# Performance work log

Hardware: AMD Instinct MI355X
Metric: run time of the kernel (lower is better)

The kernel has to match this reference:

```python
import jax, jax.numpy as jnp
from jax import lax
import numpy as np

B, N, D_MODEL = 4, 2048, 768
D_INNER = 1536      # int(2.0 * d_model)
DT_RANK = 48        # ceil(768 / 16)
EPS = 1e-5


def setup_inputs() -> dict:
    key = jax.random.key(0)
    ks = jax.random.split(key, 9)
    x = jax.random.normal(ks[0], (B, N, D_MODEL), jnp.float32)
    # BFS order: a permutation of node ids
    sorted_index = jax.random.permutation(ks[1], N).astype(jnp.int32)
    # parent BFS position of node at BFS position i, must be < i; root (i=0) has -1
    pos = jnp.arange(N)
    r = jax.random.randint(ks[2], (N,), 0, N)
    sorted_parent = jnp.where(pos == 0, -1, r % jnp.maximum(pos, 1)).astype(jnp.int32)
    s = 0.02
    in_proj_w = jax.random.normal(ks[3], (D_MODEL, 2 * D_INNER), jnp.float32) * s
    x_proj_w = jax.random.normal(ks[4], (D_INNER, DT_RANK + 2), jnp.float32) * s
    dt_proj_w = jax.random.normal(ks[5], (DT_RANK, D_INNER), jnp.float32) * (DT_RANK ** -0.5)
    # dt bias init: softplus^{-1}(dt) with dt ~ LogUniform(1e-3, 1e-1)
    dt = jnp.exp(jax.random.uniform(ks[6], (D_INNER,)) * (np.log(0.1) - np.log(0.001)) + np.log(0.001))
    dt_proj_b = (dt + jnp.log(-jnp.expm1(-dt))).astype(jnp.float32)
    A_log = jnp.zeros((D_INNER,), jnp.float32)   # log(A=1) per original init (d_state=1)
    D_param = jnp.ones((D_INNER,), jnp.float32)
    ln_gamma = jnp.ones((D_INNER,), jnp.float32)
    ln_beta = jnp.zeros((D_INNER,), jnp.float32)
    out_proj_w = jax.random.normal(ks[7], (D_INNER, D_MODEL), jnp.float32) * s
    return dict(x=x, sorted_index=sorted_index, sorted_parent=sorted_parent,
                in_proj_w=in_proj_w, x_proj_w=x_proj_w, dt_proj_w=dt_proj_w,
                dt_proj_b=dt_proj_b, A_log=A_log, D_param=D_param,
                ln_gamma=ln_gamma, ln_beta=ln_beta, out_proj_w=out_proj_w)


def _tree_ssm_recurrence(dBx, dA, sorted_index, sorted_parent):
    """h[bfs i] = dA[node(i)] * h[parent_bfs(i)] + dBx[node(i)]. Inputs (B,N,Di) node-major."""
    b, n, di = dBx.shape
    dA_bfs = jnp.take(dA, sorted_index, axis=1)    # (B,N,Di) in BFS order
    dBx_bfs = jnp.take(dBx, sorted_index, axis=1)

    def step(h_buf, inp):
        t, par, dA_t, dBx_t = inp                   # dA_t/dBx_t: (B,Di)
        h_par = h_buf[:, jnp.maximum(par, 0)]       # (B,Di) gather at parent BFS pos
        h_par = jnp.where(par < 0, jnp.zeros_like(h_par), h_par)
        h_t = dA_t * h_par + dBx_t
        return h_buf.at[:, t].set(h_t), h_t

    xs = (jnp.arange(n), sorted_parent,
          dA_bfs.transpose(1, 0, 2), dBx_bfs.transpose(1, 0, 2))
    _, h_bfs = lax.scan(step, jnp.zeros((b, n, di), dBx.dtype), xs)
    # scatter BFS-order states back to node-id order
    h = jnp.zeros((b, n, di), dBx.dtype).at[:, sorted_index].set(h_bfs.transpose(1, 0, 2))
    return h


def reference(x, sorted_index, sorted_parent, in_proj_w, x_proj_w, dt_proj_w,
              dt_proj_b, A_log, D_param, ln_gamma, ln_beta, out_proj_w):
    xz = x @ in_proj_w                              # (B,N,2*Di)
    x_inner, z = jnp.split(xz, 2, axis=-1)
    z = jax.nn.silu(z)
    x_dbl = x_inner @ x_proj_w                      # (B,N,dt_rank+2)
    dt_lr, B_ssm, C_ssm = (x_dbl[..., :DT_RANK], x_dbl[..., DT_RANK:DT_RANK + 1],
                           x_dbl[..., DT_RANK + 1:DT_RANK + 2])
    dt = jax.nn.softplus(dt_lr @ dt_proj_w + dt_proj_b)  # (B,N,Di)
    As = -jnp.exp(A_log)                            # (Di,) negative
    dA = jnp.exp(dt * As)                           # (B,N,Di) in (0,1)
    dBx = dt * B_ssm * x_inner                      # (B,N,Di)
    h = _tree_ssm_recurrence(dBx, dA, sorted_index, sorted_parent)
    y = h * C_ssm + D_param * x_inner               # (B,N,Di)
    mu = jnp.mean(y, axis=-1, keepdims=True)
    var = jnp.mean(jnp.square(y - mu), axis=-1, keepdims=True)
    y = (y - mu) * lax.rsqrt(var + EPS) * ln_gamma + ln_beta
    y = y * z
    return y @ out_proj_w                           # (B,N,D)
```

## Files before the change

kernel.cpp:

```cpp
#include <hip/hip_runtime.h>
#include <math.h>


#define ROWS 8192
#define DIN 1536
#define DMOD 768
#define NSEQ 2048
#define DTR 48

typedef __bf16 bfrag __attribute__((ext_vector_type(8)));
typedef float f4 __attribute__((ext_vector_type(4)));

__device__ __forceinline__ unsigned short f2bf(float f) {
  unsigned int u = __float_as_uint(f);
  unsigned int r = (u + 0x7fffu + ((u >> 16) & 1u)) >> 16;
  return (unsigned short)r;
}
__device__ __forceinline__ float bf2f(unsigned short h) {
  return __uint_as_float(((unsigned int)h) << 16);
}

__device__ __forceinline__ void gld_lds16(const void* g, void* l) {
  __builtin_amdgcn_global_load_lds((const __attribute__((address_space(1))) void*)g,
                                   (__attribute__((address_space(3))) void*)l, 16, 0, 0);
}

__device__ __forceinline__ void barx() {
  asm volatile("" ::: "memory");
  __builtin_amdgcn_s_barrier();
  asm volatile("" ::: "memory");
}

template <int MODE, int NCOLS>
__global__ __launch_bounds__(512, 2) void gemm_dp(
    const unsigned short* __restrict__ A, const unsigned short* __restrict__ Bt,
    void* __restrict__ C0v, void* __restrict__ C1v, int K, int ldc) {
  __shared__ unsigned short lds[2][(128 + 192) * 64];
  const int tid = threadIdx.x;
  const int w = tid >> 6, l = tid & 63;
  const int quad = l >> 4, l16 = l & 15;
  const int wr = w >> 2, wc = w & 3;
  const int h = blockIdx.x + gridDim.x * blockIdx.y;
  const int chunk = (gridDim.x * gridDim.y) >> 3;
  const int swz = (h & 7) * chunk + (h >> 3);
  const int row0 = (swz / NCOLS) * 128, col0 = (swz % NCOLS) * 192;
  const int nt = K >> 6;

  const int srow = tid >> 3;
  const int schunk = ((tid & 7) ^ (srow & 7)) * 8;
  const unsigned short* aS = A + (size_t)(row0 + srow) * K + schunk;
  const unsigned short* bS = Bt + (size_t)(col0 + srow) * K + schunk;

#define STG_A(bufi, q, kt)                                     \
  gld_lds16(aS + (size_t)((q) * 64) * K + (size_t)(kt) * 64,   \
            (char*)&lds[bufi][(q) * 4096] + w * 1024)
#define STG_B(bufi, q, kt)                                     \
  gld_lds16(bS + (size_t)((q) * 64) * K + (size_t)(kt) * 64,   \
            (char*)&lds[bufi][8192 + (q) * 4096] + w * 1024)

  const int arow = (wr * 64 + l16) * 64;
  const int brow = (wc * 48 + l16) * 64;
  int cs[2];
  cs[0] = (quad ^ (l16 & 7)) * 8;
  cs[1] = ((4 + quad) ^ (l16 & 7)) * 8;

#define RDA(m, ks) (*(const bfrag*)(const void*)(LA + arow + (m) * 1024 + cs[ks]))
#define RDB(n, ks) (*(const bfrag*)(const void*)(LB + brow + (n) * 1024 + cs[ks]))

  f4 acc[4][3];
#pragma unroll
  for (int m = 0; m < 4; m++)
#pragma unroll
    for (int n = 0; n < 3; n++) acc[m][n] = (f4){0.f, 0.f, 0.f, 0.f};

  const int kt1 = (nt > 1) ? 1 : 0;
#pragma unroll
  for (int q = 0; q < 2; q++) STG_A(0, q, 0);
#pragma unroll
  for (int q = 0; q < 3; q++) STG_B(0, q, 0);
#pragma unroll
  for (int q = 0; q < 2; q++) STG_A(1, q, kt1);
#pragma unroll
  for (int q = 0; q < 3; q++) STG_B(1, q, kt1);
  asm volatile("s_waitcnt vmcnt(5)" ::: "memory");
  barx();

  for (int t = 0; t < nt; ++t) {
    const int b = t & 1;
    const unsigned short* LA = &lds[b][0];
    const unsigned short* LB = &lds[b][8192];
    const int kA = (t + 2 < nt) ? (t + 2) : (nt - 1);
    bfrag af[4][2], bfr[3][2];

#pragma unroll
    for (int m = 0; m < 4; m++) {
      af[m][0] = RDA(m, 0);
      af[m][1] = RDA(m, 1);
    }
#pragma unroll
    for (int n = 0; n < 3; n++) {
      bfr[n][0] = RDB(n, 0);
      bfr[n][1] = RDB(n, 1);
    }
    asm volatile("s_waitcnt lgkmcnt(0)" ::: "memory");
    barx();
    STG_A(b, 0, kA);
    STG_A(b, 1, kA);
    STG_B(b, 0, kA);
    STG_B(b, 1, kA);
    STG_B(b, 2, kA);
    __builtin_amdgcn_s_setprio(1);
#pragma unroll
    for (int m = 0; m < 4; m++)
#pragma unroll
      for (int n = 0; n < 3; n++) {
        acc[m][n] = __builtin_amdgcn_mfma_f32_16x16x32_bf16(af[m][0], bfr[n][0], acc[m][n], 0, 0, 0);
        acc[m][n] = __builtin_amdgcn_mfma_f32_16x16x32_bf16(af[m][1], bfr[n][1], acc[m][n], 0, 0, 0);
      }
    __builtin_amdgcn_s_setprio(0);
    asm volatile("s_waitcnt vmcnt(5)" ::: "memory");
    barx();
  }
  asm volatile("s_waitcnt vmcnt(0)" ::: "memory");

#undef STG_A
#undef STG_B
#undef RDA
#undef RDB

  if (MODE == 0) {
    float* C0 = (float*)C0v;
    const int cb = col0 + wc * 48 + l16;
#pragma unroll
    for (int m = 0; m < 4; m++) {
      const int rb = row0 + wr * 64 + m * 16 + quad * 4;
#pragma unroll
      for (int n = 0; n < 3; n++)
#pragma unroll
        for (int r = 0; r < 4; r++)
          C0[(size_t)(rb + r) * ldc + cb + n * 16] = acc[m][n][r];
    }
  } else {
    const bool is_z = (col0 >= DIN);
    unsigned short* dst = is_z ? (unsigned short*)C1v : (unsigned short*)C0v;
    const int cb = col0 + wc * 48 + l16 - (is_z ? DIN : 0);
#pragma unroll
    for (int m = 0; m < 4; m++) {
      const int rb = row0 + wr * 64 + m * 16 + quad * 4;
#pragma unroll
      for (int n = 0; n < 3; n++)
#pragma unroll
        for (int r = 0; r < 4; r++) {
          float v = acc[m][n][r];
          if (is_z) v = v / (1.f + __expf(-v));
          dst[(size_t)(rb + r) * DIN + cb + n * 16] = f2bf(v);
        }
    }
  }
}

__global__ __launch_bounds__(1024) void prep1_kernel(
    const int* __restrict__ sidx, const int* __restrict__ spar,
    int* __restrict__ SLOT_PACK, int* __restrict__ SLOTINV,
    int* __restrict__ LSTART, int* __restrict__ NLEV,
    const float* __restrict__ x, unsigned short* __restrict__ Xbf,
    const float* __restrict__ dtw, unsigned short* __restrict__ DTWb,
    const float* __restrict__ A_log, float* __restrict__ negA) {
  const int bi = blockIdx.x;
  const int tid = threadIdx.x;
  if (bi == 0) {
    __shared__ int par[2048], idx[2048], ancA[2048], ancB[2048], rnkA[2048], rnkB[2048];
    __shared__ int dmax;
    for (int i = tid; i < 2048; i += 1024) {
      const int p = spar[i];
      par[i] = p;
      idx[i] = sidx[i];
      ancA[i] = (p < 0) ? -1 : p;
      rnkA[i] = (p < 0) ? 0 : 1;
    }
    if (tid == 0) dmax = 0;
    __syncthreads();
    for (int r = 0; r < 11; r++) {
      int* ca = (r & 1) ? ancB : ancA;
      int* cr = (r & 1) ? rnkB : rnkA;
      int* na = (r & 1) ? ancA : ancB;
      int* nr = (r & 1) ? rnkA : rnkB;
      for (int i = tid; i < 2048; i += 1024) {
        const int a = ca[i], rv = cr[i];
        if (a >= 0) {
          nr[i] = rv + cr[a];
          na[i] = ca[a];
        } else {
          nr[i] = rv;
          na[i] = a;
        }
      }
      __syncthreads();
    }
    for (int i = tid; i < 2048; i += 1024) ancA[i] = 0;
    __syncthreads();
    for (int i = tid; i < 2048; i += 1024) {
      atomicAdd(&ancA[rnkB[i]], 1);
      atomicMax(&dmax, rnkB[i]);
    }
    __syncthreads();
    for (int s = 0; s < 11; s++) {
      const int off = 1 << s;
      int* cur = (s & 1) ? ancB : ancA;
      int* nxt = (s & 1) ? ancA : ancB;
      for (int i = tid; i < 2048; i += 1024) {
        int v = cur[i];
        if (i >= off) v += cur[i - off];
        nxt[i] = v;
      }
      __syncthreads();
    }
    for (int i = tid; i < 2049; i += 1024) {
      const int v = (i == 0) ? 0 : ancB[i - 1];
      LSTART[i] = v;
      if (i < 2048) rnkA[i] = v;
    }
    if (tid == 0) NLEV[0] = dmax + 1;
    __syncthreads();
    for (int i = tid; i < 2048; i += 1024) {
      const int d = rnkB[i];
      const int slot = atomicAdd(&rnkA[d], 1);
      const int node = idx[i];
      const int p = par[i];
      const int pn = (p < 0) ? -1 : idx[p];
      SLOT_PACK[slot] = node | ((pn + 1) << 12);
      SLOTINV[node] = slot;
    }
  } else if (bi < 1 + 1536) {
    const int i = ((bi - 1) * 1024 + tid) * 4;
    const float4 v = *(const float4*)(x + i);
    union { unsigned short h[4]; uint2 u; } pk;
    pk.h[0] = f2bf(v.x);
    pk.h[1] = f2bf(v.y);
    pk.h[2] = f2bf(v.z);
    pk.h[3] = f2bf(v.w);
    *(uint2*)(Xbf + i) = pk.u;
  } else if (bi < 1 + 1536 + 96) {
    const int i = (bi - 1537) * 1024 + tid;
    const int d = i >> 6, k = i & 63;
    DTWb[i] = (k < 48) ? f2bf(dtw[(size_t)k * DIN + d]) : (unsigned short)0;
  } else {
    const int i = (bi - 1633) * 1024 + tid;
    if (i < DIN) negA[i] = -__expf(A_log[i]);
  }
}

__global__ __launch_bounds__(256) void prep2_kernel(
    const float* __restrict__ W1, unsigned short* __restrict__ W1t,
    const float* __restrict__ W2, unsigned short* __restrict__ W2t) {
  __shared__ float t[32][33];
  int idx = blockIdx.x;
  const float* W;
  unsigned short* Wt;
  int K, N, n0, k0;
  if (idx < 2304) {
    W = W1; Wt = W1t; K = DMOD; N = 2 * DIN;
    n0 = (idx % 96) * 32; k0 = (idx / 96) * 32;
  } else {
    idx -= 2304;
    W = W2; Wt = W2t; K = DIN; N = DMOD;
    n0 = (idx % 24) * 32; k0 = (idx / 24) * 32;
  }
  const int tx = threadIdx.x & 31, ty = threadIdx.x >> 5;
  for (int i = ty; i < 32; i += 8) t[i][tx] = W[(size_t)(k0 + i) * N + n0 + tx];
  __syncthreads();
  for (int i = ty; i < 32; i += 8)
    Wt[(size_t)(n0 + i) * K + k0 + tx] = f2bf(t[tx][i]);
}

__global__ __launch_bounds__(256) void cwprep_kernel(
    const float* __restrict__ W1, const float* __restrict__ xpw,
    unsigned short* __restrict__ CWt) {
  const int tid = threadIdx.x;
  const int kk = tid >> 6, lane = tid & 63;
  const int k = blockIdx.x * 4 + kk;
  float acc[50];
#pragma unroll
  for (int c = 0; c < 50; c++) acc[c] = 0.f;
  const float* wrow = W1 + (size_t)k * (2 * DIN);
  for (int j = lane; j < DIN; j += 64) {
    const float wv = wrow[j];
    const float* xr = xpw + (size_t)j * 50;
#pragma unroll
    for (int c = 0; c < 50; c++) acc[c] = fmaf(wv, xr[c], acc[c]);
  }
#pragma unroll
  for (int c = 0; c < 50; c++) {
#pragma unroll
    for (int off = 32; off >= 1; off >>= 1) acc[c] += __shfl_down(acc[c], off);
  }
  if (lane == 0) {
#pragma unroll
    for (int c = 0; c < 50; c++) CWt[(size_t)c * DMOD + k] = f2bf(acc[c]);
  }
  if (tid < 56) {
    const int c = 50 + (tid >> 2);
    const int kz = blockIdx.x * 4 + (tid & 3);
    CWt[(size_t)c * DMOD + kz] = 0;
  }
}

__global__ __launch_bounds__(256) void xdbl2_mfma(
    const unsigned short* __restrict__ Xbf, const unsigned short* __restrict__ CWt,
    unsigned short* __restrict__ DTLRb, float* __restrict__ BCv,
    float* __restrict__ CCv) {
  __shared__ unsigned short As[64 * 32];
  __shared__ unsigned short Bs[64 * 32];
  const int tid = threadIdx.x;
  const int w = tid >> 6, l = tid & 63;
  const int quad = l >> 4, l16 = l & 15;
  const int h = blockIdx.x;
  const int swz = (h & 7) * 16 + (h >> 3);
  const int row0 = swz * 64;

  f4 acc[4];
#pragma unroll
  for (int j = 0; j < 4; j++) acc[j] = (f4){0.f, 0.f, 0.f, 0.f};

  const int srow = w * 16 + (l >> 2);
  const int kcol = (((l & 3) ^ ((l >> 2) & 3)) * 8);
  const int qs = (quad ^ (l16 & 3)) * 8;

  for (int c = 0; c < 24; c++) {
    const int k0 = c * 32;
    gld_lds16(Xbf + (size_t)(row0 + srow) * DMOD + k0 + kcol,
              (char*)As + w * 1024);
    gld_lds16(CWt + (size_t)srow * DMOD + k0 + kcol, (char*)Bs + w * 1024);
    __syncthreads();
    bfrag af, bf[4];
    af = *(const bfrag*)(const void*)(As + (w * 16 + l16) * 32 + qs);
#pragma unroll
    for (int j = 0; j < 4; j++)
      bf[j] = *(const bfrag*)(const void*)(Bs + (j * 16 + l16) * 32 + qs);
#pragma unroll
    for (int j = 0; j < 4; j++)
      acc[j] = __builtin_amdgcn_mfma_f32_16x16x32_bf16(af, bf[j], acc[j], 0, 0, 0);
    __syncthreads();
  }

#pragma unroll
  for (int j = 0; j < 4; j++) {
    const int col = j * 16 + l16;
#pragma unroll
    for (int r = 0; r < 4; r++) {
      const int row = row0 + w * 16 + quad * 4 + r;
      const float v = acc[j][r];
      DTLRb[(size_t)row * 64 + col] = f2bf(v);
      if (col == 48) BCv[row] = v;
      else if (col == 49) CCv[row] = v;
    }
  }
}

__global__ __launch_bounds__(256) void dt_gemm(
    const unsigned short* __restrict__ DTLRb, const unsigned short* __restrict__ DTWb,
    const float* __restrict__ bias, const float* __restrict__ negA,
    const float* __restrict__ BCv, const unsigned short* __restrict__ XI,
    const int* __restrict__ SLOTINV,
    unsigned short* __restrict__ DAp, unsigned short* __restrict__ DBXp) {
  __shared__ unsigned short As[2][64 * 32];
  __shared__ unsigned short Bs[2][128 * 32];
  __shared__ int sinv[64];
  __shared__ float bcs[64];
  const int tid = threadIdx.x;
  const int w = tid >> 6, l = tid & 63;
  const int quad = l >> 4, l16 = l & 15;
  const int wrow = (w >> 1) * 32, wcol = (w & 1) * 64;
  const int h = blockIdx.x + 12 * blockIdx.y;
  const int swz = (h & 7) * 192 + (h >> 3);
  const int row0 = (swz / 12) * 64, col0 = (swz % 12) * 128;
  const int p0 = row0 & (NSEQ - 1);
  const int bbase = row0 & ~(NSEQ - 1);
  const int srow = w * 16 + (l >> 2);
  const int koff = (((l & 3) ^ ((l >> 2) & 3)) * 8);
  const int qs = (quad ^ (l16 & 3)) * 8;

#pragma unroll
  for (int c = 0; c < 2; c++) {
    gld_lds16(DTLRb + (size_t)(row0 + srow) * 64 + c * 32 + koff,
              (char*)As[c] + w * 1024);
#pragma unroll
    for (int r = 0; r < 2; r++)
      gld_lds16(DTWb + (size_t)(col0 + srow + r * 64) * 64 + c * 32 + koff,
                (char*)Bs[c] + r * 4096 + w * 1024);
  }
  if (tid < 64) {
    sinv[tid] = SLOTINV[p0 + tid];
    bcs[tid] = BCv[row0 + tid];
  }
  __syncthreads();

  f4 acc[2][4];
#pragma unroll
  for (int i = 0; i < 2; i++)
#pragma unroll
    for (int j = 0; j < 4; j++) acc[i][j] = (f4){0.f, 0.f, 0.f, 0.f};

#pragma unroll
  for (int c = 0; c < 2; c++) {
    bfrag af[2], bf[4];
#pragma unroll
    for (int i = 0; i < 2; i++)
      af[i] = *(const bfrag*)(const void*)(As[c] + (wrow + i * 16 + l16) * 32 + qs);
#pragma unroll
    for (int j = 0; j < 4; j++)
      bf[j] = *(const bfrag*)(const void*)(Bs[c] + (wcol + j * 16 + l16) * 32 + qs);
#pragma unroll
    for (int i = 0; i < 2; i++)
#pragma unroll
      for (int j = 0; j < 4; j++)
        acc[i][j] = __builtin_amdgcn_mfma_f32_16x16x32_bf16(af[i], bf[j], acc[i][j], 0, 0, 0);
  }

  float bj[4], aj[4];
#pragma unroll
  for (int j = 0; j < 4; j++) {
    const int d = col0 + wcol + j * 16 + l16;
    bj[j] = bias[d];
    aj[j] = negA[d];
  }
#pragma unroll
  for (int i = 0; i < 2; i++) {
#pragma unroll
    for (int r = 0; r < 4; r++) {
      const int row_l = wrow + i * 16 + quad * 4 + r;
      const int row = row0 + row_l;
      const float bc = bcs[row_l];
      const size_t rp = (size_t)(bbase + sinv[row_l]) * DIN;
#pragma unroll
      for (int j = 0; j < 4; j++) {
        const int d = col0 + wcol + j * 16 + l16;
        const float s = acc[i][j][r] + bj[j];
        const float sp = fmaxf(s, 0.f) + __logf(1.f + __expf(-fabsf(s)));
        const float xi = bf2f(XI[(size_t)row * DIN + d]);
        DAp[rp + d] = f2bf(__expf(sp * aj[j]));
        DBXp[rp + d] = f2bf(sp * bc * xi);
      }
    }
  }
}

__global__ __launch_bounds__(256) void recur_kernel(
    const unsigned short* __restrict__ DAp, const unsigned short* __restrict__ DBXp,
    unsigned short* __restrict__ Hb,
    const int* __restrict__ SLOT_PACK, const int* __restrict__ LSTART,
    const int* __restrict__ NLEV) {
  __shared__ unsigned short hl[NSEQ * 16];
  __shared__ int spack[NSEQ];
  __shared__ int lst[258];
  const int tid = threadIdx.x;
  const int bid = blockIdx.x;
  const int logical = (bid & 7) * 48 + (bid >> 3);
  const int c8a = logical * 2;
  const int b = c8a / 192;
  const int d8a = c8a % 192;
  const int nlev = NLEV[0];
  for (int i = tid; i < NSEQ; i += 256) spack[i] = SLOT_PACK[i];
  const int nl = (nlev + 1 < 258) ? nlev + 1 : 258;
  for (int i = tid; i < nl; i += 256) lst[i] = LSTART[i];
  __syncthreads();

  for (int L = 0; L < nlev; L++) {
    const int s0 = (L < 257) ? lst[L] : LSTART[L];
    const int s1 = (L + 1 < 258) ? lst[L + 1] : LSTART[L + 1];
    const int items = (s1 - s0) * 2;
    for (int it = tid; it < items; it += 256) {
      const int s = s0 + (it >> 1);
      const int ch = it & 1;
      const size_t goff = (size_t)(b * NSEQ + s) * DIN + (d8a + ch) * 8;
      union { uint4 u; unsigned short h[8]; } da, dbx, hpu, hvu;
      da.u = *(const uint4*)(DAp + goff);
      dbx.u = *(const uint4*)(DBXp + goff);
      const int pk = spack[s];
      const int node = pk & 4095;
      const int pn = (pk >> 12) - 1;
      float hp[8];
      if (pn >= 0) {
        hpu.u = *(const uint4*)(hl + pn * 16 + ch * 8);
#pragma unroll
        for (int e = 0; e < 8; e++) hp[e] = bf2f(hpu.h[e]);
      } else {
#pragma unroll
        for (int e = 0; e < 8; e++) hp[e] = 0.f;
      }
#pragma unroll
      for (int e = 0; e < 8; e++) {
        const float hv = fmaf(bf2f(da.h[e]), hp[e], bf2f(dbx.h[e]));
        hvu.h[e] = f2bf(hv);
      }
      *(uint4*)(hl + node * 16 + ch * 8) = hvu.u;
    }
    __syncthreads();
  }

  for (int i = tid; i < NSEQ * 2; i += 256) {
    const int node = i >> 1, ch = i & 1;
    *(uint4*)(Hb + (size_t)(b * NSEQ + node) * DIN + (d8a + ch) * 8) =
        *(const uint4*)(hl + node * 16 + ch * 8);
  }
}

__global__ __launch_bounds__(192) void ln_kernel(
    const unsigned short* __restrict__ Hb, const float* __restrict__ CCv,
    const unsigned short* __restrict__ XI, const float* __restrict__ Dp,
    const float* __restrict__ gamma, const float* __restrict__ beta,
    const unsigned short* __restrict__ Z, unsigned short* __restrict__ YLN) {
  const int row = blockIdx.x;
  const int tid = threadIdx.x;
  const int d8 = tid * 8;
  const float C = CCv[row];
  const size_t base = (size_t)row * DIN + d8;
  union U { uint4 u; unsigned short h[8]; };
  U hu, xu;
  hu.u = *(const uint4*)(Hb + base);
  xu.u = *(const uint4*)(XI + base);
  float dp[8];
  *(float4*)(dp) = *(const float4*)(Dp + d8);
  *(float4*)(dp + 4) = *(const float4*)(Dp + d8 + 4);
  float y[8];
  float s = 0.f, s2 = 0.f;
#pragma unroll
  for (int e = 0; e < 8; e++) {
    const float v = fmaf(bf2f(hu.h[e]), C, dp[e] * bf2f(xu.h[e]));
    y[e] = v;
    s += v;
    s2 = fmaf(v, v, s2);
  }
#pragma unroll
  for (int off = 32; off >= 1; off >>= 1) {
    s += __shfl_down(s, off);
    s2 += __shfl_down(s2, off);
  }
  __shared__ float rs[3], rs2[3];
  const int w = tid >> 6;
  if ((tid & 63) == 0) {
    rs[w] = s;
    rs2[w] = s2;
  }
  __syncthreads();
  const float ts = rs[0] + rs[1] + rs[2];
  const float ts2 = rs2[0] + rs2[1] + rs2[2];
  const float mu = ts * (1.f / 1536.f);
  const float var = ts2 * (1.f / 1536.f) - mu * mu;
  const float inv = rsqrtf(var + 1e-5f);
  float g[8], bb[8];
  *(float4*)(g) = *(const float4*)(gamma + d8);
  *(float4*)(g + 4) = *(const float4*)(gamma + d8 + 4);
  *(float4*)(bb) = *(const float4*)(beta + d8);
  *(float4*)(bb + 4) = *(const float4*)(beta + d8 + 4);
  U zu, out;
  zu.u = *(const uint4*)(Z + base);
#pragma unroll
  for (int e = 0; e < 8; e++) {
    const float o = (y[e] - mu) * inv * g[e] + bb[e];
    out.h[e] = f2bf(o * bf2f(zu.h[e]));
  }
  *(uint4*)(YLN + base) = out.u;
}

extern "C" void kernel_launch(void* const* d_in, const int* in_sizes, int n_in,
                              void* d_out, int out_size, void* d_ws, size_t ws_size,
                              hipStream_t stream) {
  const float* x = (const float*)d_in[0];
  const int* sidx = (const int*)d_in[1];
  const int* spar = (const int*)d_in[2];
  const float* in_proj = (const float*)d_in[3];
  const float* x_proj = (const float*)d_in[4];
  const float* dt_proj = (const float*)d_in[5];
  const float* dt_b = (const float*)d_in[6];
  const float* A_log = (const float*)d_in[7];
  const float* Dp = (const float*)d_in[8];
  const float* gamma = (const float*)d_in[9];
  const float* beta = (const float*)d_in[10];
  const float* out_proj = (const float*)d_in[11];
  float* out = (float*)d_out;

  char* p = (char*)d_ws;
  const size_t RC = (size_t)ROWS * DIN;
  unsigned short* XI = (unsigned short*)p;   p += RC * 2;
  unsigned short* Z = (unsigned short*)p;    p += RC * 2;
  unsigned short* DAp = (unsigned short*)p;  p += RC * 2;
  unsigned short* DBXp = (unsigned short*)p; p += RC * 2;
  unsigned short* Hb = (unsigned short*)p;   p += RC * 2;
  unsigned short* DTLRb = (unsigned short*)p; p += (size_t)ROWS * 64 * 2;
  float* BCv = (float*)p;                    p += ROWS * 4;
  float* CCv = (float*)p;                    p += ROWS * 4;
  float* negA = (float*)p;                   p += DIN * 4;
  unsigned short* Xbf = (unsigned short*)p;  p += (size_t)ROWS * DMOD * 2;
  unsigned short* W1t = (unsigned short*)p;  p += (size_t)2 * DIN * DMOD * 2;
  unsigned short* W2t = (unsigned short*)p;  p += (size_t)DMOD * DIN * 2;
  unsigned short* CWt = (unsigned short*)p;  p += (size_t)64 * DMOD * 2;
  unsigned short* DTWb = (unsigned short*)p; p += (size_t)DIN * 64 * 2;
  int* ipart = (int*)p;
  int* SLOT_PACK = ipart;
  int* SLOTINV = ipart + 2048;
  int* LSTART = ipart + 4096;
  int* NLEV = ipart + 4096 + 2049;
  unsigned short* YLN = DAp;

  prep1_kernel<<<1635, 1024, 0, stream>>>(sidx, spar, SLOT_PACK, SLOTINV,
                                          LSTART, NLEV, x, Xbf, dt_proj, DTWb,
                                          A_log, negA);
  prep2_kernel<<<3456, 256, 0, stream>>>(in_proj, W1t, out_proj, W2t);
  cwprep_kernel<<<192, 256, 0, stream>>>(in_proj, x_proj, CWt);
  xdbl2_mfma<<<128, 256, 0, stream>>>(Xbf, CWt, DTLRb, BCv, CCv);
  gemm_dp<1, 16><<<dim3(16, 64), 512, 0, stream>>>(Xbf, W1t, XI, Z, DMOD, 0);
  dt_gemm<<<dim3(12, 128), 256, 0, stream>>>(DTLRb, DTWb, dt_b, negA, BCv, XI,
                                             SLOTINV, DAp, DBXp);
  recur_kernel<<<384, 256, 0, stream>>>(DAp, DBXp, Hb, SLOT_PACK, LSTART, NLEV);
  ln_kernel<<<ROWS, 192, 0, stream>>>(Hb, CCv, XI, Dp, gamma, beta, Z, YLN);
  gemm_dp<0, 4><<<dim3(4, 64), 512, 0, stream>>>(YLN, W2t, out, nullptr, DIN, DMOD);
}
```

Measured before the change: 284.8 us.

## Double-buffer xdbl MFMA GEMM with smaller tiles and restructure cwprep weight fold

Reworks the x_dbl GEMM into 32-row tiles with K=64 steps, a 2x2 wave layout and double-buffered LDS loads issued via global_load_lds. This overlaps memory with MFMA and doubles the grid size. It also rewrites the W1·x_proj fold so each lane owns one output column over 4 rows, which removes the 50-way shuffle reductions but leaves only 48 blocks doing a serial 1536-long dot product. The wait counts and barrier ordering are delicate.

```diff
diff --git a/kernel.cpp b/kernel.cpp
--- a/kernel.cpp
+++ b/kernel.cpp
@@ -277,79 +277,120 @@
     const float* __restrict__ W1, const float* __restrict__ xpw,
     unsigned short* __restrict__ CWt) {
   const int tid = threadIdx.x;
-  const int kk = tid >> 6, lane = tid & 63;
-  const int k = blockIdx.x * 4 + kk;
-  float acc[50];
-#pragma unroll
-  for (int c = 0; c < 50; c++) acc[c] = 0.f;
-  const float* wrow = W1 + (size_t)k * (2 * DIN);
-  for (int j = lane; j < DIN; j += 64) {
-    const float wv = wrow[j];
-    const float* xr = xpw + (size_t)j * 50;
-#pragma unroll
-    for (int c = 0; c < 50; c++) acc[c] = fmaf(wv, xr[c], acc[c]);
-  }
-#pragma unroll
-  for (int c = 0; c < 50; c++) {
-#pragma unroll
-    for (int off = 32; off >= 1; off >>= 1) acc[c] += __shfl_down(acc[c], off);
-  }
-  if (lane == 0) {
-#pragma unroll
-    for (int c = 0; c < 50; c++) CWt[(size_t)c * DMOD + k] = f2bf(acc[c]);
-  }
-  if (tid < 56) {
-    const int c = 50 + (tid >> 2);
-    const int kz = blockIdx.x * 4 + (tid & 3);
-    CWt[(size_t)c * DMOD + kz] = 0;
-  }
-}
-
-__global__ __launch_bounds__(256) void xdbl2_mfma(
+  const int w = tid >> 6, lane = tid & 63;
+  const int k0 = (blockIdx.x * 4 + w) * 4;
+  const float* r0 = W1 + (size_t)(k0 + 0) * (2 * DIN);
+  const float* r1 = W1 + (size_t)(k0 + 1) * (2 * DIN);
+  const float* r2 = W1 + (size_t)(k0 + 2) * (2 * DIN);
+  const float* r3 = W1 + (size_t)(k0 + 3) * (2 * DIN);
+  float a0 = 0.f, a1 = 0.f, a2 = 0.f, a3 = 0.f;
+  if (lane < 50) {
+    const float* xc = xpw + lane;
+    for (int j = 0; j < DIN; j += 4) {
+#pragma unroll
+      for (int u = 0; u < 4; u++) {
+        const float xv = xc[(size_t)(j + u) * 50];
+        a0 = fmaf(r0[j + u], xv, a0);
+        a1 = fmaf(r1[j + u], xv, a1);
+        a2 = fmaf(r2[j + u], xv, a2);
+        a3 = fmaf(r3[j + u], xv, a3);
+      }
+    }
+    CWt[(size_t)lane * DMOD + k0 + 0] = f2bf(a0);
+    CWt[(size_t)lane * DMOD + k0 + 1] = f2bf(a1);
+    CWt[(size_t)lane * DMOD + k0 + 2] = f2bf(a2);
+    CWt[(size_t)lane * DMOD + k0 + 3] = f2bf(a3);
+  } else {
+    CWt[(size_t)lane * DMOD + k0 + 0] = 0;
+    CWt[(size_t)lane * DMOD + k0 + 1] = 0;
+    CWt[(size_t)lane * DMOD + k0 + 2] = 0;
+    CWt[(size_t)lane * DMOD + k0 + 3] = 0;
+  }
+}
+
+__global__ __launch_bounds__(256, 2) void xdbl2_mfma(
     const unsigned short* __restrict__ Xbf, const unsigned short* __restrict__ CWt,
     unsigned short* __restrict__ DTLRb, float* __restrict__ BCv,
     float* __restrict__ CCv) {
-  __shared__ unsigned short As[64 * 32];
-  __shared__ unsigned short Bs[64 * 32];
+  __shared__ unsigned short lds[2][(32 + 64) * 64];
   const int tid = threadIdx.x;
   const int w = tid >> 6, l = tid & 63;
   const int quad = l >> 4, l16 = l & 15;
+  const int wr = w >> 1, wc = w & 1;
   const int h = blockIdx.x;
-  const int swz = (h & 7) * 16 + (h >> 3);
-  const int row0 = swz * 64;
-
-  f4 acc[4];
-#pragma unroll
-  for (int j = 0; j < 4; j++) acc[j] = (f4){0.f, 0.f, 0.f, 0.f};
-
-  const int srow = w * 16 + (l >> 2);
-  const int kcol = (((l & 3) ^ ((l >> 2) & 3)) * 8);
-  const int qs = (quad ^ (l16 & 3)) * 8;
-
-  for (int c = 0; c < 24; c++) {
-    const int k0 = c * 32;
-    gld_lds16(Xbf + (size_t)(row0 + srow) * DMOD + k0 + kcol,
-              (char*)As + w * 1024);
-    gld_lds16(CWt + (size_t)srow * DMOD + k0 + kcol, (char*)Bs + w * 1024);
-    __syncthreads();
-    bfrag af, bf[4];
-    af = *(const bfrag*)(const void*)(As + (w * 16 + l16) * 32 + qs);
-#pragma unroll
-    for (int j = 0; j < 4; j++)
-      bf[j] = *(const bfrag*)(const void*)(Bs + (j * 16 + l16) * 32 + qs);
-#pragma unroll
-    for (int j = 0; j < 4; j++)
-      acc[j] = __builtin_amdgcn_mfma_f32_16x16x32_bf16(af, bf[j], acc[j], 0, 0, 0);
-    __syncthreads();
-  }
-
-#pragma unroll
-  for (int j = 0; j < 4; j++) {
-    const int col = j * 16 + l16;
+  const int swz = (h & 7) * 32 + (h >> 3);
+  const int row0 = swz * 32;
+  const int nt = 12;
+
+  const int srow = tid >> 3;
+  const int schunk = ((tid & 7) ^ (srow & 7)) * 8;
+  const unsigned short* aS = Xbf + (size_t)(row0 + srow) * DMOD + schunk;
+  const unsigned short* bS = CWt + (size_t)srow * DMOD + schunk;
+
+#define XSTG_A(bufi, kt)                                        \
+  gld_lds16(aS + (size_t)(kt) * 64, (char*)&lds[bufi][0] + w * 1024)
+#define XSTG_B(bufi, q, kt)                                     \
+  gld_lds16(bS + (size_t)((q) * 32) * DMOD + (size_t)(kt) * 64, \
+            (char*)&lds[bufi][2048 + (q) * 2048] + w * 1024)
+
+  const int arow = (wr * 16 + l16) * 64;
+  int cs[2];
+  cs[0] = (quad ^ (l16 & 7)) * 8;
+  cs[1] = ((4 + quad) ^ (l16 & 7)) * 8;
+
+  f4 acc[2];
+  acc[0] = (f4){0.f, 0.f, 0.f, 0.f};
+  acc[1] = (f4){0.f, 0.f, 0.f, 0.f};
+
+  XSTG_A(0, 0);
+  XSTG_B(0, 0, 0);
+  XSTG_B(0, 1, 0);
+  XSTG_A(1, 1);
+  XSTG_B(1, 0, 1);
+  XSTG_B(1, 1, 1);
+  asm volatile("s_waitcnt vmcnt(3)" ::: "memory");
+  barx();
+
+  for (int t = 0; t < nt; ++t) {
+    const int b = t & 1;
+    const unsigned short* L = &lds[b][0];
+    const int kA = (t + 2 < nt) ? (t + 2) : (nt - 1);
+    bfrag af[2], bf[2][2];
+    af[0] = *(const bfrag*)(const void*)(L + arow + cs[0]);
+    af[1] = *(const bfrag*)(const void*)(L + arow + cs[1]);
+#pragma unroll
+    for (int n = 0; n < 2; n++) {
+      const int brow = 2048 + (wc * 32 + n * 16 + l16) * 64;
+      bf[n][0] = *(const bfrag*)(const void*)(L + brow + cs[0]);
+      bf[n][1] = *(const bfrag*)(const void*)(L + brow + cs[1]);
+    }
+    asm volatile("s_waitcnt lgkmcnt(0)" ::: "memory");
+    barx();
+    XSTG_A(b, kA);
+    XSTG_B(b, 0, kA);
+    XSTG_B(b, 1, kA);
+    __builtin_amdgcn_s_setprio(1);
+#pragma unroll
+    for (int n = 0; n < 2; n++) {
+      acc[n] = __builtin_amdgcn_mfma_f32_16x16x32_bf16(af[0], bf[n][0], acc[n], 0, 0, 0);
+      acc[n] = __builtin_amdgcn_mfma_f32_16x16x32_bf16(af[1], bf[n][1], acc[n], 0, 0, 0);
+    }
+    __builtin_amdgcn_s_setprio(0);
+    asm volatile("s_waitcnt vmcnt(3)" ::: "memory");
+    barx();
+  }
+  asm volatile("s_waitcnt vmcnt(0)" ::: "memory");
+
+#undef XSTG_A
+#undef XSTG_B
+
+#pragma unroll
+  for (int n = 0; n < 2; n++) {
+    const int col = wc * 32 + n * 16 + l16;
 #pragma unroll
     for (int r = 0; r < 4; r++) {
-      const int row = row0 + w * 16 + quad * 4 + r;
-      const float v = acc[j][r];
+      const int row = row0 + wr * 16 + quad * 4 + r;
+      const float v = acc[n][r];
       DTLRb[(size_t)row * 64 + col] = f2bf(v);
       if (col == 48) BCv[row] = v;
       else if (col == 49) CCv[row] = v;
@@ -607,8 +648,8 @@
                                           LSTART, NLEV, x, Xbf, dt_proj, DTWb,
                                           A_log, negA);
   prep2_kernel<<<3456, 256, 0, stream>>>(in_proj, W1t, out_proj, W2t);
-  cwprep_kernel<<<192, 256, 0, stream>>>(in_proj, x_proj, CWt);
-  xdbl2_mfma<<<128, 256, 0, stream>>>(Xbf, CWt, DTLRb, BCv, CCv);
+  cwprep_kernel<<<48, 256, 0, stream>>>(in_proj, x_proj, CWt);
+  xdbl2_mfma<<<256, 256, 0, stream>>>(Xbf, CWt, DTLRb, BCv, CCv);
   gemm_dp<1, 16><<<dim3(16, 64), 512, 0, stream>>>(Xbf, W1t, XI, Z, DMOD, 0);
   dt_gemm<<<dim3(12, 128), 256, 0, stream>>>(DTLRb, DTWb, dt_b, negA, BCv, XI,
                                              SLOTINV, DAp, DBXp);
```

Result: slower. 426.2 us (+49.6%).
